# Kernel optimization log

Hardware: AMD Instinct MI355X
Metric: run time of the kernel (lower is better)

## Reference

```python
import jax, jax.numpy as jnp
import numpy as np

INPUT_SIZE = 512
LABEL_NUM = 8
OUTPUT_SIZE = 64
H1 = 1024  # shared bottom width
H2 = 512   # expert hidden width
B = 8192


def setup_inputs() -> dict:
    key = jax.random.key(0)
    ks = jax.random.split(key, 8)
    s_in = 1.0 / np.sqrt(INPUT_SIZE)
    s_h1 = 1.0 / np.sqrt(H1)
    s_h2 = 1.0 / np.sqrt(H2)
    return {
        "input": jax.random.normal(ks[0], (B, INPUT_SIZE), dtype=jnp.float32),
        "category": jax.random.randint(ks[1], (B,), 0, LABEL_NUM, dtype=jnp.int32),
        # shared bottom Linear(input_size, 1024): stored as [in, out]
        "W_in": jax.random.uniform(ks[2], (INPUT_SIZE, H1), jnp.float32, -s_in, s_in),
        "b_in": jax.random.uniform(ks[3], (H1,), jnp.float32, -s_in, s_in),
        # per-expert Linear(1024, 512) stacked over experts
        "W1": jax.random.uniform(ks[4], (LABEL_NUM, H1, H2), jnp.float32, -s_h1, s_h1),
        "b1": jax.random.uniform(ks[5], (LABEL_NUM, H2), jnp.float32, -s_h1, s_h1),
        # per-expert Linear(512, output_size) stacked over experts
        "W2": jax.random.uniform(ks[6], (LABEL_NUM, H2, OUTPUT_SIZE), jnp.float32, -s_h2, s_h2),
        "b2": jax.random.uniform(ks[7], (LABEL_NUM, OUTPUT_SIZE), jnp.float32, -s_h2, s_h2),
    }


def reference(input, category, W_in, b_in, W1, b1, W2, b2):
    # Shared bottom: Linear + ELU -> [B, H1]
    mid = jax.nn.elu(input @ W_in + b_in)
    # Run all experts densely, then hard-select per-sample expert output.
    # (Faithful to per-sample hard routing; small expert count makes this clean.)
    h = jax.nn.elu(jnp.einsum("bd,edh->beh", mid, W1) + b1[None, :, :])  # [B,E,H2]
    out_all = jnp.einsum("beh,eho->beo", h, W2) + b2[None, :, :]          # [B,E,O]
    # gather the chosen expert's output for each sample
    out = jnp.take_along_axis(out_all, category[:, None, None].astype(jnp.int32).repeat(1, axis=1), axis=1)
    return out[:, 0, :]  # [B, O]
```

## Files before the change

### kernel.cpp

```cpp
#include <hip/hip_runtime.h>

typedef unsigned short u16;
typedef unsigned int u32;
typedef __bf16 bf16x8 __attribute__((ext_vector_type(8)));
typedef float f32x4 __attribute__((ext_vector_type(4)));

#define GLD_LDS(gptr, lptr) \
  __builtin_amdgcn_global_load_lds((const __attribute__((address_space(1))) void*)(gptr), \
                                   (__attribute__((address_space(3))) void*)(lptr), 16, 0, 0)

__device__ __forceinline__ u16 f2b(float f) {
  union { __bf16 h; u16 u; } v; v.h = (__bf16)f; return v.u;
}
__device__ __forceinline__ float elu1(float v) {
  return v > 0.f ? v : (__expf(v) - 1.f);
}

__device__ void transpose_tile(float (*tbuf)[65], const float* __restrict__ src,
                               u16* __restrict__ dst, int R, int C, int tr, int tc,
                               size_t zoff) {
  const int tid = threadIdx.x;
  const float* sp = src + zoff + (size_t)(tr * 64) * C + tc * 64;
#pragma unroll
  for (int i = 0; i < 4; i++) {
    const int rr = (tid >> 4) + i * 16, f = tid & 15;
    float4 v = *reinterpret_cast<const float4*>(sp + (size_t)rr * C + f * 4);
    tbuf[rr][f * 4 + 0] = v.x; tbuf[rr][f * 4 + 1] = v.y;
    tbuf[rr][f * 4 + 2] = v.z; tbuf[rr][f * 4 + 3] = v.w;
  }
  __syncthreads();
  u16* dp = dst + zoff + (size_t)(tc * 64) * R + tr * 64;
#pragma unroll
  for (int i = 0; i < 4; i++) {
    const int u = tid + i * 256;
    const int c = u >> 4, rq = u & 15;
    ushort4 w;
    w.x = f2b(tbuf[rq * 4 + 0][c]); w.y = f2b(tbuf[rq * 4 + 1][c]);
    w.z = f2b(tbuf[rq * 4 + 2][c]); w.w = f2b(tbuf[rq * 4 + 3][c]);
    *reinterpret_cast<ushort4*>(dp + (size_t)c * R + rq * 4) = w;
  }
}

__device__ void hist_body(int rb, const int* __restrict__ cat, int* __restrict__ cnts) {
  __shared__ int c8[8];
  const int tid = threadIdx.x;
  if (tid < 8) c8[tid] = 0;
  __syncthreads();
  if (tid < 128) atomicAdd(&c8[cat[rb * 128 + tid]], 1);
  __syncthreads();
  if (tid < 8) cnts[rb * 8 + tid] = c8[tid];
}

__device__ void scatter_body(int rb, const int* __restrict__ cat,
                             const int* __restrict__ cnts,
                             int* __restrict__ list, int* __restrict__ off) {
  __shared__ int lc[512];
  __shared__ int lcur[8];
  __shared__ int starts[8];
  const int tid = threadIdx.x;
  lc[tid] = cnts[tid];
  lc[tid + 256] = cnts[tid + 256];
  if (tid < 8) lcur[tid] = 0;
  __syncthreads();
  if (tid < 8) {
    const int c = tid;
    int base = 0;
    for (int cc = 0; cc < c; cc++) {
      int s = 0;
      for (int b = 0; b < 64; b++) s += lc[b * 8 + cc];
      base += s;
    }
    int pre = 0;
    for (int b = 0; b < rb; b++) pre += lc[b * 8 + c];
    starts[c] = base + pre;
    if (rb == 0) {
      off[c] = base;
      if (c == 7) {
        int s = 0;
        for (int b = 0; b < 64; b++) s += lc[b * 8 + 7];
        off[8] = base + s;
      }
    }
  }
  __syncthreads();
  if (tid < 128) {
    const int idx = rb * 128 + tid;
    const int c = cat[idx];
    const int r = atomicAdd(&lcur[c], 1);
    list[starts[c] + r] = idx;
  }
}

__global__ __launch_bounds__(256) void wsmall(const float* __restrict__ W_in,
                                              const int* __restrict__ cat,
                                              u16* __restrict__ o0, int* __restrict__ cnts) {
  __shared__ float tbuf[64][65];
  const int bid = blockIdx.x;
  if (bid >= 128) { hist_body(bid - 128, cat, cnts); return; }
  transpose_tile(tbuf, W_in, o0, 512, 1024, bid >> 4, bid & 15, 0);
}


template<int LAYER, int BN, int K, int N>
__global__ __launch_bounds__(256, 4) void gemm_t(
    const float* __restrict__ Xf, const u16* __restrict__ A,
    const u16* __restrict__ Bw, const float* __restrict__ bias,
    const int* __restrict__ list, const int* __restrict__ off,
    u16* __restrict__ outb, float* __restrict__ outf,
    const int* __restrict__ cat, const int* __restrict__ cnts,
    int* __restrict__ wlist, int* __restrict__ woff,
    const float* __restrict__ Wc1, const float* __restrict__ Wc2,
    u16* __restrict__ o1, u16* __restrict__ o2,
    const float* __restrict__ b2r) {
  struct GBuf { alignas(16) u16 As[2][2048]; alignas(16) u16 Bs[2][BN * 32]; };
  __shared__ union SM {
    GBuf g;
    float tbuf[64][65];
    u16 ht[64 * 136];
  } sm;

  const int tid = threadIdx.x;

  if constexpr (LAYER == 1) {
    if (blockIdx.y == 8) {
      if (blockIdx.x < 64) scatter_body(blockIdx.x, cat, cnts, wlist, woff);
      return;
    }
    if (blockIdx.y >= 9) {
      if (blockIdx.y <= 16) {
        const int t = (blockIdx.y - 9) * 128 + blockIdx.x;
        const int z = t >> 7, rem = t & 127;
        transpose_tile(sm.tbuf, Wc1, o1, 1024, 512, rem >> 3, rem & 7,
                       (size_t)z * 1024 * 512);
      } else if (blockIdx.y == 17) {
        if (blockIdx.x < 64) {
          const int t = blockIdx.x, z = t >> 3;
          transpose_tile(sm.tbuf, Wc2, o2, 512, 64, t & 7, 0, (size_t)z * 512 * 64);
        }
      } else {
        const int r = blockIdx.x * 64 + (tid >> 2);
        const int co = (tid & 3) * 16;
        const int c = cat[r];
#pragma unroll
        for (int q = 0; q < 4; q++) {
          float4 v = *reinterpret_cast<const float4*>(b2r + c * 64 + co + q * 4);
          *reinterpret_cast<float4*>(outf + (size_t)r * 64 + co + q * 4) = v;
        }
      }
      return;
    }
  }

  int tidx, col0;
  if constexpr (LAYER == 1) {
    const int orig = blockIdx.y * 128 + blockIdx.x;
    const int work = (orig & 7) * 128 + (orig >> 3);
    tidx = work >> 3;
    col0 = (work & 7) * BN;
  } else {
    const int orig = blockIdx.y * 136 + blockIdx.x;
    const int work = (orig & 7) * 68 + (orig >> 3);
    tidx = work >> 2;
    col0 = (work & 3) * BN;
  }

  const int wave = tid >> 6, lane = tid & 63;

  int e = 0, start = 0, cnt = 0, rowbase;
  if constexpr (LAYER == 1) {
    rowbase = tidx * 64;
  } else {
    int t = tidx;
    int found = -1;
    for (e = 0; e < 8; e++) {
      int tiles = (off[e + 1] - off[e] + 63) >> 6;
      if (t < tiles) { found = e; break; }
      t -= tiles;
    }
    if (found < 0) return;
    start = off[e];
    cnt = off[e + 1] - start;
    rowbase = t * 64;
  }

  const int srow = tid >> 2, skc = tid & 3;
  const int kxs = (skc ^ (srow & 3)) * 8;

  const float* ax = nullptr;
  const u16* a_src = nullptr;
  if constexpr (LAYER == 1) {
    ax = Xf + (size_t)(rowbase + srow) * K + kxs;
  } else {
    int gr = list[start + min(rowbase + srow, cnt - 1)];
    a_src = A + (size_t)gr * K + kxs;
  }
  const u16* Bbase = Bw + (LAYER == 1 ? (size_t)0 : (size_t)e * N * K);
  const u16* b_src0 = Bbase + (size_t)(col0 + srow) * K + kxs;
  const u16* b_src1 = Bbase + (size_t)(col0 + 64 + srow) * K + kxs;

  const int wbase = wave * 512;

  constexpr int NR = BN / 32;
  const int wy = wave & 1, wx = wave >> 1;
  const int fr = lane & 15, kg = lane >> 4;
  const int kx = (kg ^ (fr & 3)) * 8;
  const int ar0 = (wy * 32 + fr) * 32 + kx;
  const int br0 = (wx * (BN / 2) + fr) * 32 + kx;

  f32x4 acc[2][NR] = {};

  float4 va0, va1;
  auto LOAD_A1 = [&](int t) {
    va0 = *reinterpret_cast<const float4*>(ax + t * 32);
    va1 = *reinterpret_cast<const float4*>(ax + t * 32 + 4);
  };
  auto WRITE_A1 = [&](int buf) {
    uint4 w;
    w.x = (u32)f2b(va0.x) | ((u32)f2b(va0.y) << 16);
    w.y = (u32)f2b(va0.z) | ((u32)f2b(va0.w) << 16);
    w.z = (u32)f2b(va1.x) | ((u32)f2b(va1.y) << 16);
    w.w = (u32)f2b(va1.z) | ((u32)f2b(va1.w) << 16);
    *reinterpret_cast<uint4*>(&sm.g.As[buf][srow * 32 + skc * 8]) = w;
  };
  auto COMPUTE = [&](int buf) {
    bf16x8 af[2], bfv[NR];
#pragma unroll
    for (int m = 0; m < 2; m++) af[m] = *(const bf16x8*)&sm.g.As[buf][ar0 + m * 16 * 32];
#pragma unroll
    for (int n = 0; n < NR; n++) bfv[n] = *(const bf16x8*)&sm.g.Bs[buf][br0 + n * 16 * 32];
#pragma unroll
    for (int m = 0; m < 2; m++)
#pragma unroll
      for (int n = 0; n < NR; n++)
        acc[m][n] = __builtin_amdgcn_mfma_f32_16x16x32_bf16(af[m], bfv[n], acc[m][n], 0, 0, 0);
  };

  constexpr int NK = K / 32;
  if constexpr (LAYER == 1) LOAD_A1(0);
  else GLD_LDS(a_src, &sm.g.As[0][wbase]);
  GLD_LDS(b_src0, &sm.g.Bs[0][wbase]);
  if constexpr (BN == 128) GLD_LDS(b_src1, &sm.g.Bs[0][2048 + wbase]);
  if constexpr (LAYER == 1) WRITE_A1(0);
  __syncthreads();

  for (int it = 0; it < NK; ++it) {
    const int cur = it & 1;
    const int nxt = cur ^ 1;
    if (it + 1 < NK) {
      const int kt = (it + 1) * 32;
      if constexpr (LAYER == 1) LOAD_A1(it + 1);
      else GLD_LDS(a_src + kt, &sm.g.As[nxt][wbase]);
      GLD_LDS(b_src0 + kt, &sm.g.Bs[nxt][wbase]);
      if constexpr (BN == 128) GLD_LDS(b_src1 + kt, &sm.g.Bs[nxt][2048 + wbase]);
    }
    COMPUTE(cur);
    if constexpr (LAYER == 1) { if (it + 1 < NK) WRITE_A1(nxt); }
    __syncthreads();
  }

  if constexpr (LAYER == 1) {
#pragma unroll
    for (int n = 0; n < NR; n++) {
      const int col = col0 + wx * (BN / 2) + n * 16 + fr;
      const float bc = bias[col];
#pragma unroll
      for (int m = 0; m < 2; m++) {
        const int rloc = wy * 32 + m * 16 + kg * 4;
#pragma unroll
        for (int j = 0; j < 4; j++)
          outb[(size_t)(rowbase + rloc + j) * N + col] = f2b(elu1(acc[m][n][j] + bc));
      }
    }
  } else {
#pragma unroll
    for (int n = 0; n < NR; n++) {
      const int lcol = wx * 64 + n * 16 + fr;
      const float bc = bias[e * N + col0 + lcol];
#pragma unroll
      for (int m = 0; m < 2; m++) {
        const int rl = wy * 32 + m * 16 + kg * 4;
#pragma unroll
        for (int j = 0; j < 4; j++)
          sm.ht[(rl + j) * 136 + lcol] = f2b(elu1(acc[m][n][j] + bc));
      }
    }
    __syncthreads();

    const u16* w2p = o2 + (size_t)e * 64 * 512 + col0;
    f32x4 po[2][2] = {};
#pragma unroll
    for (int ks = 0; ks < 4; ks++) {
      bf16x8 pa[2], pb[2];
#pragma unroll
      for (int m = 0; m < 2; m++)
        pa[m] = *(const bf16x8*)&sm.ht[(wy * 32 + m * 16 + fr) * 136 + ks * 32 + kg * 8];
#pragma unroll
      for (int n = 0; n < 2; n++)
        pb[n] = *(const bf16x8*)&w2p[(size_t)(wx * 32 + n * 16 + fr) * 512 + ks * 32 + kg * 8];
#pragma unroll
      for (int m = 0; m < 2; m++)
#pragma unroll
        for (int n = 0; n < 2; n++)
          po[m][n] = __builtin_amdgcn_mfma_f32_16x16x32_bf16(pa[m], pb[n], po[m][n], 0, 0, 0);
    }
#pragma unroll
    for (int n = 0; n < 2; n++) {
      const int oc = wx * 32 + n * 16 + fr;
#pragma unroll
      for (int m = 0; m < 2; m++) {
        const int sl0 = rowbase + wy * 32 + m * 16 + kg * 4;
#pragma unroll
        for (int j = 0; j < 4; j++) {
          const int slot = sl0 + j;
          if (slot < cnt)
            atomicAdd(&outf[(size_t)list[start + slot] * 64 + oc], po[m][n][j]);
        }
      }
    }
  }
}


extern "C" void kernel_launch(void* const* d_in, const int* in_sizes, int n_in,
                              void* d_out, int out_size, void* d_ws, size_t ws_size,
                              hipStream_t stream) {
  const float* x    = (const float*)d_in[0];
  const int*   cat  = (const int*)d_in[1];
  const float* W_in = (const float*)d_in[2];
  const float* b_in = (const float*)d_in[3];
  const float* W1   = (const float*)d_in[4];
  const float* b1   = (const float*)d_in[5];
  const float* W2   = (const float*)d_in[6];
  const float* b2   = (const float*)d_in[7];
  float* out = (float*)d_out;

  char* p = (char*)d_ws;
  u16* midb = (u16*)p; p += (size_t)8192 * 1024 * 2;
  u16* wtin = (u16*)p; p += (size_t)1024 * 512 * 2;
  u16* w1t  = (u16*)p; p += (size_t)8 * 512 * 1024 * 2;
  u16* w2t  = (u16*)p; p += (size_t)8 * 64 * 512 * 2;
  int* list = (int*)p; p += (size_t)8192 * 4;
  int* off  = (int*)p; p += 64;
  int* cnts = (int*)p; p += 64 * 8 * 4;

  wsmall<<<192, 256, 0, stream>>>(W_in, cat, wtin, cnts);

  gemm_t<1, 128, 512, 1024><<<dim3(128, 19), 256, 0, stream>>>(
      x, nullptr, wtin, b_in, nullptr, nullptr, midb, out,
      cat, cnts, list, off, W1, W2, w1t, w2t, b2);

  gemm_t<2, 128, 1024, 512><<<dim3(136, 4), 256, 0, stream>>>(
      nullptr, midb, w1t, b1, list, off, nullptr, out,
      nullptr, nullptr, nullptr, nullptr, nullptr, nullptr, nullptr, w2t, nullptr);
}
```

Baseline: 59.78 us.

## Move W1/W2 transposes and bias init into the prep kernel

Moves the per-expert W1/W2 bf16 transpose tiles and the b2 output initialisation out of the layer-1 GEMM launch and into the first small prep kernel, which grows from 192 to 1408 blocks. The layer-1 GEMM grid shrinks to only GEMM and scatter blocks, and dropping the tbuf member from its shared-memory union may lower LDS use. The cost is that the transpose work no longer overlaps with the layer-1 GEMM. It now runs serially before it, in a kernel that was previously tiny.

```diff
diff --git a/kernel.cpp b/kernel.cpp
--- a/kernel.cpp
+++ b/kernel.cpp
@@ -92,10 +92,37 @@
 }
 
 __global__ __launch_bounds__(256) void wsmall(const float* __restrict__ W_in,
+                                              const float* __restrict__ W1,
+                                              const float* __restrict__ W2,
                                               const int* __restrict__ cat,
-                                              u16* __restrict__ o0, int* __restrict__ cnts) {
+                                              const float* __restrict__ b2,
+                                              u16* __restrict__ o0, u16* __restrict__ o1,
+                                              u16* __restrict__ o2, int* __restrict__ cnts,
+                                              float* __restrict__ out) {
   __shared__ float tbuf[64][65];
-  const int bid = blockIdx.x;
+  const int bid = blockIdx.x, tid = threadIdx.x;
+  if (bid >= 1280) {
+    const int r = (bid - 1280) * 64 + (tid >> 2);
+    const int co = (tid & 3) * 16;
+    const int c = cat[r];
+#pragma unroll
+    for (int q = 0; q < 4; q++) {
+      float4 v = *reinterpret_cast<const float4*>(b2 + c * 64 + co + q * 4);
+      *reinterpret_cast<float4*>(out + (size_t)r * 64 + co + q * 4) = v;
+    }
+    return;
+  }
+  if (bid >= 1216) {
+    const int t = bid - 1216, z = t >> 3;
+    transpose_tile(tbuf, W2, o2, 512, 64, t & 7, 0, (size_t)z * 512 * 64);
+    return;
+  }
+  if (bid >= 192) {
+    const int t = bid - 192;
+    const int z = t >> 7, rem = t & 127;
+    transpose_tile(tbuf, W1, o1, 1024, 512, rem >> 3, rem & 7, (size_t)z * 1024 * 512);
+    return;
+  }
   if (bid >= 128) { hist_body(bid - 128, cat, cnts); return; }
   transpose_tile(tbuf, W_in, o0, 512, 1024, bid >> 4, bid & 15, 0);
 }
@@ -109,13 +136,10 @@
     u16* __restrict__ outb, float* __restrict__ outf,
     const int* __restrict__ cat, const int* __restrict__ cnts,
     int* __restrict__ wlist, int* __restrict__ woff,
-    const float* __restrict__ Wc1, const float* __restrict__ Wc2,
-    u16* __restrict__ o1, u16* __restrict__ o2,
-    const float* __restrict__ b2r) {
+    const u16* __restrict__ o2) {
   struct GBuf { alignas(16) u16 As[2][2048]; alignas(16) u16 Bs[2][BN * 32]; };
   __shared__ union SM {
     GBuf g;
-    float tbuf[64][65];
     u16 ht[64 * 136];
   } sm;
 
@@ -124,29 +148,6 @@
   if constexpr (LAYER == 1) {
     if (blockIdx.y == 8) {
       if (blockIdx.x < 64) scatter_body(blockIdx.x, cat, cnts, wlist, woff);
-      return;
-    }
-    if (blockIdx.y >= 9) {
-      if (blockIdx.y <= 16) {
-        const int t = (blockIdx.y - 9) * 128 + blockIdx.x;
-        const int z = t >> 7, rem = t & 127;
-        transpose_tile(sm.tbuf, Wc1, o1, 1024, 512, rem >> 3, rem & 7,
-                       (size_t)z * 1024 * 512);
-      } else if (blockIdx.y == 17) {
-        if (blockIdx.x < 64) {
-          const int t = blockIdx.x, z = t >> 3;
-          transpose_tile(sm.tbuf, Wc2, o2, 512, 64, t & 7, 0, (size_t)z * 512 * 64);
-        }
-      } else {
-        const int r = blockIdx.x * 64 + (tid >> 2);
-        const int co = (tid & 3) * 16;
-        const int c = cat[r];
-#pragma unroll
-        for (int q = 0; q < 4; q++) {
-          float4 v = *reinterpret_cast<const float4*>(b2r + c * 64 + co + q * 4);
-          *reinterpret_cast<float4*>(outf + (size_t)r * 64 + co + q * 4) = v;
-        }
-      }
       return;
     }
   }
@@ -343,13 +344,13 @@
   int* off  = (int*)p; p += 64;
   int* cnts = (int*)p; p += 64 * 8 * 4;
 
-  wsmall<<<192, 256, 0, stream>>>(W_in, cat, wtin, cnts);
-
-  gemm_t<1, 128, 512, 1024><<<dim3(128, 19), 256, 0, stream>>>(
+  wsmall<<<1408, 256, 0, stream>>>(W_in, W1, W2, cat, b2, wtin, w1t, w2t, cnts, out);
+
+  gemm_t<1, 128, 512, 1024><<<dim3(128, 9), 256, 0, stream>>>(
       x, nullptr, wtin, b_in, nullptr, nullptr, midb, out,
-      cat, cnts, list, off, W1, W2, w1t, w2t, b2);
+      cat, cnts, list, off, nullptr);
 
   gemm_t<2, 128, 1024, 512><<<dim3(136, 4), 256, 0, stream>>>(
       nullptr, midb, w1t, b1, list, off, nullptr, out,
-      nullptr, nullptr, nullptr, nullptr, nullptr, nullptr, nullptr, w2t, nullptr);
-}
+      nullptr, nullptr, nullptr, nullptr, w2t);
+}
```

After: 61.62 us. 1.03x slower.

## Drop the W_in pre-transpose kernel; load fp32 W_in directly into layer-1 GEMM

Applied to the files above, without the earlier changes.

Removes the separate wsmall launch that transposed W_in to bf16 and built per-block histograms. The layer-1 GEMM now reads fp32 W_in columns directly, converts them to bf16 in registers and writes them into swizzled LDS. Routing is also collapsed into a single block that counts and scatters all 8192 samples. This saves one kernel launch and a global round trip, at the cost of strided scalar global loads for B in layer 1 and a serialized single-block routing step.

```diff
diff --git a/kernel.cpp b/kernel.cpp
--- a/kernel.cpp
+++ b/kernel.cpp
@@ -11,6 +11,9 @@
 
 __device__ __forceinline__ u16 f2b(float f) {
   union { __bf16 h; u16 u; } v; v.h = (__bf16)f; return v.u;
+}
+__device__ __forceinline__ u32 pk2(float a, float b) {
+  return (u32)f2b(a) | ((u32)f2b(b) << 16);
 }
 __device__ __forceinline__ float elu1(float v) {
   return v > 0.f ? v : (__expf(v) - 1.f);
@@ -41,74 +44,38 @@
   }
 }
 
-__device__ void hist_body(int rb, const int* __restrict__ cat, int* __restrict__ cnts) {
-  __shared__ int c8[8];
+__device__ void route_body(const int* __restrict__ cat, int* __restrict__ list,
+                           int* __restrict__ off) {
+  __shared__ int cnt[8], cur[8], offs[9];
   const int tid = threadIdx.x;
-  if (tid < 8) c8[tid] = 0;
-  __syncthreads();
-  if (tid < 128) atomicAdd(&c8[cat[rb * 128 + tid]], 1);
-  __syncthreads();
-  if (tid < 8) cnts[rb * 8 + tid] = c8[tid];
-}
-
-__device__ void scatter_body(int rb, const int* __restrict__ cat,
-                             const int* __restrict__ cnts,
-                             int* __restrict__ list, int* __restrict__ off) {
-  __shared__ int lc[512];
-  __shared__ int lcur[8];
-  __shared__ int starts[8];
-  const int tid = threadIdx.x;
-  lc[tid] = cnts[tid];
-  lc[tid + 256] = cnts[tid + 256];
-  if (tid < 8) lcur[tid] = 0;
-  __syncthreads();
-  if (tid < 8) {
-    const int c = tid;
-    int base = 0;
-    for (int cc = 0; cc < c; cc++) {
-      int s = 0;
-      for (int b = 0; b < 64; b++) s += lc[b * 8 + cc];
-      base += s;
-    }
-    int pre = 0;
-    for (int b = 0; b < rb; b++) pre += lc[b * 8 + c];
-    starts[c] = base + pre;
-    if (rb == 0) {
-      off[c] = base;
-      if (c == 7) {
-        int s = 0;
-        for (int b = 0; b < 64; b++) s += lc[b * 8 + 7];
-        off[8] = base + s;
-      }
-    }
-  }
-  __syncthreads();
-  if (tid < 128) {
-    const int idx = rb * 128 + tid;
-    const int c = cat[idx];
-    const int r = atomicAdd(&lcur[c], 1);
-    list[starts[c] + r] = idx;
-  }
-}
-
-__global__ __launch_bounds__(256) void wsmall(const float* __restrict__ W_in,
-                                              const int* __restrict__ cat,
-                                              u16* __restrict__ o0, int* __restrict__ cnts) {
-  __shared__ float tbuf[64][65];
-  const int bid = blockIdx.x;
-  if (bid >= 128) { hist_body(bid - 128, cat, cnts); return; }
-  transpose_tile(tbuf, W_in, o0, 512, 1024, bid >> 4, bid & 15, 0);
+  if (tid < 8) cnt[tid] = 0;
+  __syncthreads();
+  for (int i = tid; i < 8192; i += 256) atomicAdd(&cnt[cat[i]], 1);
+  __syncthreads();
+  if (tid == 0) {
+    int s = 0;
+    for (int e = 0; e < 8; e++) { offs[e] = s; s += cnt[e]; }
+    offs[8] = s;
+  }
+  __syncthreads();
+  if (tid < 8) cur[tid] = offs[tid];
+  if (tid < 9) off[tid] = offs[tid];
+  __syncthreads();
+  for (int i = tid; i < 8192; i += 256) {
+    int c = cat[i];
+    list[atomicAdd(&cur[c], 1)] = i;
+  }
 }
 
 
 template<int LAYER, int BN, int K, int N>
 __global__ __launch_bounds__(256, 4) void gemm_t(
-    const float* __restrict__ Xf, const u16* __restrict__ A,
-    const u16* __restrict__ Bw, const float* __restrict__ bias,
+    const float* __restrict__ Xf, const float* __restrict__ Wf,
+    const u16* __restrict__ A, const u16* __restrict__ Bw,
+    const float* __restrict__ bias,
     const int* __restrict__ list, const int* __restrict__ off,
     u16* __restrict__ outb, float* __restrict__ outf,
-    const int* __restrict__ cat, const int* __restrict__ cnts,
-    int* __restrict__ wlist, int* __restrict__ woff,
+    const int* __restrict__ cat, int* __restrict__ wlist, int* __restrict__ woff,
     const float* __restrict__ Wc1, const float* __restrict__ Wc2,
     u16* __restrict__ o1, u16* __restrict__ o2,
     const float* __restrict__ b2r) {
@@ -123,7 +90,7 @@
 
   if constexpr (LAYER == 1) {
     if (blockIdx.y == 8) {
-      if (blockIdx.x < 64) scatter_body(blockIdx.x, cat, cnts, wlist, woff);
+      if (blockIdx.x == 0) route_body(cat, wlist, woff);
       return;
     }
     if (blockIdx.y >= 9) {
@@ -188,15 +155,17 @@
 
   const float* ax = nullptr;
   const u16* a_src = nullptr;
+  const u16* b_src0 = nullptr;
+  const u16* b_src1 = nullptr;
   if constexpr (LAYER == 1) {
     ax = Xf + (size_t)(rowbase + srow) * K + kxs;
   } else {
     int gr = list[start + min(rowbase + srow, cnt - 1)];
     a_src = A + (size_t)gr * K + kxs;
-  }
-  const u16* Bbase = Bw + (LAYER == 1 ? (size_t)0 : (size_t)e * N * K);
-  const u16* b_src0 = Bbase + (size_t)(col0 + srow) * K + kxs;
-  const u16* b_src1 = Bbase + (size_t)(col0 + 64 + srow) * K + kxs;
+    const u16* Bbase = Bw + (size_t)e * N * K;
+    b_src0 = Bbase + (size_t)(col0 + srow) * K + kxs;
+    b_src1 = Bbase + (size_t)(col0 + 64 + srow) * K + kxs;
+  }
 
   const int wbase = wave * 512;
 
@@ -210,17 +179,38 @@
   f32x4 acc[2][NR] = {};
 
   float4 va0, va1;
+  u32 bw[2][4];
+  const int bcl = wave * 32 + (lane & 31);
+  const int bg0 = lane >> 5;
+
   auto LOAD_A1 = [&](int t) {
     va0 = *reinterpret_cast<const float4*>(ax + t * 32);
     va1 = *reinterpret_cast<const float4*>(ax + t * 32 + 4);
   };
   auto WRITE_A1 = [&](int buf) {
     uint4 w;
-    w.x = (u32)f2b(va0.x) | ((u32)f2b(va0.y) << 16);
-    w.y = (u32)f2b(va0.z) | ((u32)f2b(va0.w) << 16);
-    w.z = (u32)f2b(va1.x) | ((u32)f2b(va1.y) << 16);
-    w.w = (u32)f2b(va1.z) | ((u32)f2b(va1.w) << 16);
+    w.x = pk2(va0.x, va0.y); w.y = pk2(va0.z, va0.w);
+    w.z = pk2(va1.x, va1.y); w.w = pk2(va1.z, va1.w);
     *reinterpret_cast<uint4*>(&sm.g.As[buf][srow * 32 + skc * 8]) = w;
+  };
+  auto LOAD_B1 = [&](int t) {
+#pragma unroll
+    for (int h = 0; h < 2; h++) {
+      const int kg2 = bg0 + 2 * h;
+      const float* wp = Wf + (size_t)(t * 32 + kg2 * 8) * N + col0 + bcl;
+#pragma unroll
+      for (int q = 0; q < 4; q++)
+        bw[h][q] = pk2(wp[(size_t)(2 * q) * N], wp[(size_t)(2 * q + 1) * N]);
+    }
+  };
+  auto WRITE_B1 = [&](int buf) {
+#pragma unroll
+    for (int h = 0; h < 2; h++) {
+      const int kg2 = bg0 + 2 * h;
+      const int s = kg2 ^ (bcl & 3);
+      uint4 w; w.x = bw[h][0]; w.y = bw[h][1]; w.z = bw[h][2]; w.w = bw[h][3];
+      *reinterpret_cast<uint4*>(&sm.g.Bs[buf][bcl * 32 + s * 8]) = w;
+    }
   };
   auto COMPUTE = [&](int buf) {
     bf16x8 af[2], bfv[NR];
@@ -236,11 +226,14 @@
   };
 
   constexpr int NK = K / 32;
-  if constexpr (LAYER == 1) LOAD_A1(0);
-  else GLD_LDS(a_src, &sm.g.As[0][wbase]);
-  GLD_LDS(b_src0, &sm.g.Bs[0][wbase]);
-  if constexpr (BN == 128) GLD_LDS(b_src1, &sm.g.Bs[0][2048 + wbase]);
-  if constexpr (LAYER == 1) WRITE_A1(0);
+  if constexpr (LAYER == 1) {
+    LOAD_A1(0); LOAD_B1(0);
+    WRITE_A1(0); WRITE_B1(0);
+  } else {
+    GLD_LDS(a_src, &sm.g.As[0][wbase]);
+    GLD_LDS(b_src0, &sm.g.Bs[0][wbase]);
+    GLD_LDS(b_src1, &sm.g.Bs[0][2048 + wbase]);
+  }
   __syncthreads();
 
   for (int it = 0; it < NK; ++it) {
@@ -248,13 +241,18 @@
     const int nxt = cur ^ 1;
     if (it + 1 < NK) {
       const int kt = (it + 1) * 32;
-      if constexpr (LAYER == 1) LOAD_A1(it + 1);
-      else GLD_LDS(a_src + kt, &sm.g.As[nxt][wbase]);
-      GLD_LDS(b_src0 + kt, &sm.g.Bs[nxt][wbase]);
-      if constexpr (BN == 128) GLD_LDS(b_src1 + kt, &sm.g.Bs[nxt][2048 + wbase]);
+      if constexpr (LAYER == 1) {
+        LOAD_A1(it + 1); LOAD_B1(it + 1);
+      } else {
+        GLD_LDS(a_src + kt, &sm.g.As[nxt][wbase]);
+        GLD_LDS(b_src0 + kt, &sm.g.Bs[nxt][wbase]);
+        GLD_LDS(b_src1 + kt, &sm.g.Bs[nxt][2048 + wbase]);
+      }
     }
     COMPUTE(cur);
-    if constexpr (LAYER == 1) { if (it + 1 < NK) WRITE_A1(nxt); }
+    if constexpr (LAYER == 1) {
+      if (it + 1 < NK) { WRITE_A1(nxt); WRITE_B1(nxt); }
+    }
     __syncthreads();
   }
 
@@ -336,20 +334,16 @@
 
   char* p = (char*)d_ws;
   u16* midb = (u16*)p; p += (size_t)8192 * 1024 * 2;
-  u16* wtin = (u16*)p; p += (size_t)1024 * 512 * 2;
   u16* w1t  = (u16*)p; p += (size_t)8 * 512 * 1024 * 2;
   u16* w2t  = (u16*)p; p += (size_t)8 * 64 * 512 * 2;
   int* list = (int*)p; p += (size_t)8192 * 4;
   int* off  = (int*)p; p += 64;
-  int* cnts = (int*)p; p += 64 * 8 * 4;
-
-  wsmall<<<192, 256, 0, stream>>>(W_in, cat, wtin, cnts);
 
   gemm_t<1, 128, 512, 1024><<<dim3(128, 19), 256, 0, stream>>>(
-      x, nullptr, wtin, b_in, nullptr, nullptr, midb, out,
-      cat, cnts, list, off, W1, W2, w1t, w2t, b2);
+      x, W_in, nullptr, nullptr, b_in, nullptr, nullptr, midb, out,
+      cat, list, off, W1, W2, w1t, w2t, b2);
 
   gemm_t<2, 128, 1024, 512><<<dim3(136, 4), 256, 0, stream>>>(
-      nullptr, midb, w1t, b1, list, off, nullptr, out,
-      nullptr, nullptr, nullptr, nullptr, nullptr, nullptr, nullptr, w2t, nullptr);
-}
+      nullptr, nullptr, midb, w1t, b1, list, off, nullptr, out,
+      nullptr, nullptr, nullptr, nullptr, nullptr, nullptr, w2t, nullptr);
+}
```

Result: slower. 62.45 us (+4.5%).

## Enlarge layer-1 GEMM tile to 128x128 and repack auxiliary blocks into fewer rows

Applied to the files above, without the earlier changes.

Layer-1 GEMM now uses a 128-row M tile (each thread converts two rows of fp32 input to bf16), halving the number of GEMM blocks and raising operand reuse per block. The auxiliary work (scatter, weight transposes, bias prefill) is packed into fewer grid rows with the bias fill now doing 128 rows per block. Launch bounds drop to 3 waves per SIMD for layer 1 to accommodate the larger accumulator register footprint, trading occupancy for reuse.

```diff
diff --git a/kernel.cpp b/kernel.cpp
--- a/kernel.cpp
+++ b/kernel.cpp
@@ -102,7 +102,7 @@
 
 
 template<int LAYER, int BN, int K, int N>
-__global__ __launch_bounds__(256, 4) void gemm_t(
+__global__ __launch_bounds__(256, (LAYER == 1) ? 3 : 4) void gemm_t(
     const float* __restrict__ Xf, const u16* __restrict__ A,
     const u16* __restrict__ Bw, const float* __restrict__ bias,
     const int* __restrict__ list, const int* __restrict__ off,
@@ -112,7 +112,10 @@
     const float* __restrict__ Wc1, const float* __restrict__ Wc2,
     u16* __restrict__ o1, u16* __restrict__ o2,
     const float* __restrict__ b2r) {
-  struct GBuf { alignas(16) u16 As[2][2048]; alignas(16) u16 Bs[2][BN * 32]; };
+  constexpr int BM = (LAYER == 1) ? 128 : 64;
+  constexpr int MR = BM / 32;
+  constexpr int NR = BN / 32;
+  struct GBuf { alignas(16) u16 As[2][BM * 32]; alignas(16) u16 Bs[2][BN * 32]; };
   __shared__ union SM {
     GBuf g;
     float tbuf[64][65];
@@ -122,27 +125,23 @@
   const int tid = threadIdx.x;
 
   if constexpr (LAYER == 1) {
-    if (blockIdx.y == 8) {
-      if (blockIdx.x < 64) scatter_body(blockIdx.x, cat, cnts, wlist, woff);
-      return;
-    }
-    if (blockIdx.y >= 9) {
-      if (blockIdx.y <= 16) {
-        const int t = (blockIdx.y - 9) * 128 + blockIdx.x;
+    if (blockIdx.y >= 4) {
+      if (blockIdx.y == 4) {
+        if (blockIdx.x < 64) scatter_body(blockIdx.x, cat, cnts, wlist, woff);
+      } else if (blockIdx.y <= 12) {
+        const int t = (blockIdx.y - 5) * 128 + blockIdx.x;
         const int z = t >> 7, rem = t & 127;
         transpose_tile(sm.tbuf, Wc1, o1, 1024, 512, rem >> 3, rem & 7,
                        (size_t)z * 1024 * 512);
-      } else if (blockIdx.y == 17) {
-        if (blockIdx.x < 64) {
-          const int t = blockIdx.x, z = t >> 3;
-          transpose_tile(sm.tbuf, Wc2, o2, 512, 64, t & 7, 0, (size_t)z * 512 * 64);
-        }
+      } else if (blockIdx.x < 64) {
+        const int t = blockIdx.x, z = t >> 3;
+        transpose_tile(sm.tbuf, Wc2, o2, 512, 64, t & 7, 0, (size_t)z * 512 * 64);
       } else {
-        const int r = blockIdx.x * 64 + (tid >> 2);
-        const int co = (tid & 3) * 16;
+        const int r = (blockIdx.x - 64) * 128 + (tid >> 1);
+        const int co = (tid & 1) * 32;
         const int c = cat[r];
 #pragma unroll
-        for (int q = 0; q < 4; q++) {
+        for (int q = 0; q < 8; q++) {
           float4 v = *reinterpret_cast<const float4*>(b2r + c * 64 + co + q * 4);
           *reinterpret_cast<float4*>(outf + (size_t)r * 64 + co + q * 4) = v;
         }
@@ -154,7 +153,7 @@
   int tidx, col0;
   if constexpr (LAYER == 1) {
     const int orig = blockIdx.y * 128 + blockIdx.x;
-    const int work = (orig & 7) * 128 + (orig >> 3);
+    const int work = (orig & 7) * 64 + (orig >> 3);
     tidx = work >> 3;
     col0 = (work & 7) * BN;
   } else {
@@ -168,7 +167,7 @@
 
   int e = 0, start = 0, cnt = 0, rowbase;
   if constexpr (LAYER == 1) {
-    rowbase = tidx * 64;
+    rowbase = tidx * BM;
   } else {
     int t = tidx;
     int found = -1;
@@ -186,10 +185,12 @@
   const int srow = tid >> 2, skc = tid & 3;
   const int kxs = (skc ^ (srow & 3)) * 8;
 
-  const float* ax = nullptr;
+  const float* ax0 = nullptr;
+  const float* ax1 = nullptr;
   const u16* a_src = nullptr;
   if constexpr (LAYER == 1) {
-    ax = Xf + (size_t)(rowbase + srow) * K + kxs;
+    ax0 = Xf + (size_t)(rowbase + srow) * K + kxs;
+    ax1 = ax0 + (size_t)64 * K;
   } else {
     int gr = list[start + min(rowbase + srow, cnt - 1)];
     a_src = A + (size_t)gr * K + kxs;
@@ -200,19 +201,20 @@
 
   const int wbase = wave * 512;
 
-  constexpr int NR = BN / 32;
   const int wy = wave & 1, wx = wave >> 1;
   const int fr = lane & 15, kg = lane >> 4;
   const int kx = (kg ^ (fr & 3)) * 8;
-  const int ar0 = (wy * 32 + fr) * 32 + kx;
+  const int ar0 = (wy * (BM / 2) + fr) * 32 + kx;
   const int br0 = (wx * (BN / 2) + fr) * 32 + kx;
 
-  f32x4 acc[2][NR] = {};
-
-  float4 va0, va1;
+  f32x4 acc[MR][NR] = {};
+
+  float4 va0, va1, va2, va3;
   auto LOAD_A1 = [&](int t) {
-    va0 = *reinterpret_cast<const float4*>(ax + t * 32);
-    va1 = *reinterpret_cast<const float4*>(ax + t * 32 + 4);
+    va0 = *reinterpret_cast<const float4*>(ax0 + t * 32);
+    va1 = *reinterpret_cast<const float4*>(ax0 + t * 32 + 4);
+    va2 = *reinterpret_cast<const float4*>(ax1 + t * 32);
+    va3 = *reinterpret_cast<const float4*>(ax1 + t * 32 + 4);
   };
   auto WRITE_A1 = [&](int buf) {
     uint4 w;
@@ -221,15 +223,21 @@
     w.z = (u32)f2b(va1.x) | ((u32)f2b(va1.y) << 16);
     w.w = (u32)f2b(va1.z) | ((u32)f2b(va1.w) << 16);
     *reinterpret_cast<uint4*>(&sm.g.As[buf][srow * 32 + skc * 8]) = w;
+    uint4 u;
+    u.x = (u32)f2b(va2.x) | ((u32)f2b(va2.y) << 16);
+    u.y = (u32)f2b(va2.z) | ((u32)f2b(va2.w) << 16);
+    u.z = (u32)f2b(va3.x) | ((u32)f2b(va3.y) << 16);
+    u.w = (u32)f2b(va3.z) | ((u32)f2b(va3.w) << 16);
+    *reinterpret_cast<uint4*>(&sm.g.As[buf][(64 + srow) * 32 + skc * 8]) = u;
   };
   auto COMPUTE = [&](int buf) {
-    bf16x8 af[2], bfv[NR];
-#pragma unroll
-    for (int m = 0; m < 2; m++) af[m] = *(const bf16x8*)&sm.g.As[buf][ar0 + m * 16 * 32];
+    bf16x8 af[MR], bfv[NR];
+#pragma unroll
+    for (int m = 0; m < MR; m++) af[m] = *(const bf16x8*)&sm.g.As[buf][ar0 + m * 16 * 32];
 #pragma unroll
     for (int n = 0; n < NR; n++) bfv[n] = *(const bf16x8*)&sm.g.Bs[buf][br0 + n * 16 * 32];
 #pragma unroll
-    for (int m = 0; m < 2; m++)
+    for (int m = 0; m < MR; m++)
 #pragma unroll
       for (int n = 0; n < NR; n++)
         acc[m][n] = __builtin_amdgcn_mfma_f32_16x16x32_bf16(af[m], bfv[n], acc[m][n], 0, 0, 0);
@@ -239,7 +247,7 @@
   if constexpr (LAYER == 1) LOAD_A1(0);
   else GLD_LDS(a_src, &sm.g.As[0][wbase]);
   GLD_LDS(b_src0, &sm.g.Bs[0][wbase]);
-  if constexpr (BN == 128) GLD_LDS(b_src1, &sm.g.Bs[0][2048 + wbase]);
+  GLD_LDS(b_src1, &sm.g.Bs[0][2048 + wbase]);
   if constexpr (LAYER == 1) WRITE_A1(0);
   __syncthreads();
 
@@ -251,7 +259,7 @@
       if constexpr (LAYER == 1) LOAD_A1(it + 1);
       else GLD_LDS(a_src + kt, &sm.g.As[nxt][wbase]);
       GLD_LDS(b_src0 + kt, &sm.g.Bs[nxt][wbase]);
-      if constexpr (BN == 128) GLD_LDS(b_src1 + kt, &sm.g.Bs[nxt][2048 + wbase]);
+      GLD_LDS(b_src1 + kt, &sm.g.Bs[nxt][2048 + wbase]);
     }
     COMPUTE(cur);
     if constexpr (LAYER == 1) { if (it + 1 < NK) WRITE_A1(nxt); }
@@ -264,8 +272,8 @@
       const int col = col0 + wx * (BN / 2) + n * 16 + fr;
       const float bc = bias[col];
 #pragma unroll
-      for (int m = 0; m < 2; m++) {
-        const int rloc = wy * 32 + m * 16 + kg * 4;
+      for (int m = 0; m < MR; m++) {
+        const int rloc = wy * (BM / 2) + m * 16 + kg * 4;
 #pragma unroll
         for (int j = 0; j < 4; j++)
           outb[(size_t)(rowbase + rloc + j) * N + col] = f2b(elu1(acc[m][n][j] + bc));
@@ -277,7 +285,7 @@
       const int lcol = wx * 64 + n * 16 + fr;
       const float bc = bias[e * N + col0 + lcol];
 #pragma unroll
-      for (int m = 0; m < 2; m++) {
+      for (int m = 0; m < MR; m++) {
         const int rl = wy * 32 + m * 16 + kg * 4;
 #pragma unroll
         for (int j = 0; j < 4; j++)
@@ -345,7 +353,7 @@
 
   wsmall<<<192, 256, 0, stream>>>(W_in, cat, wtin, cnts);
 
-  gemm_t<1, 128, 512, 1024><<<dim3(128, 19), 256, 0, stream>>>(
+  gemm_t<1, 128, 512, 1024><<<dim3(128, 14), 256, 0, stream>>>(
       x, nullptr, wtin, b_in, nullptr, nullptr, midb, out,
       cat, cnts, list, off, W1, W2, w1t, w2t, b2);
 
```

After: 61.10 us. 1.02x slower.
